# Kernel tuning notes

Hardware: AMD Instinct MI355X
Metric: run time of the kernel (lower is better)

## Reference

```python
import jax, jax.numpy as jnp
import numpy as np
import math

D_MODEL, N_HEADS, D_HEAD = 768, 12, 64
INIT_RANGE = 0.02
ROPE_BASE = 10000.0


def _rope_cos_sin(seq_len, d_head, dtype=jnp.float32):
    # theta_j = base^(-2j/d), positions m -> angles [T, d/2]
    inv_freq = 1.0 / (ROPE_BASE ** (jnp.arange(0, d_head, 2, dtype=jnp.float32) / d_head))
    ang = jnp.arange(seq_len, dtype=jnp.float32)[:, None] * inv_freq[None, :]
    return jnp.cos(ang).astype(dtype), jnp.sin(ang).astype(dtype)


def _apply_rope(x, cos, sin):
    # x: [b, t, h, d]; rotate consecutive (even, odd) pairs as complex numbers
    xr, xi = x[..., 0::2], x[..., 1::2]
    c = cos[None, :, None, :]
    s = sin[None, :, None, :]
    out_r = xr * c - xi * s
    out_i = xr * s + xi * c
    return jnp.stack([out_r, out_i], axis=-1).reshape(x.shape)


def setup_inputs() -> dict:
    key = jax.random.key(0)
    ks = jax.random.split(key, 5)
    B, T = 2, 2048
    x = jax.random.normal(ks[0], (B, T, D_MODEL), dtype=jnp.float32)
    W_Q = INIT_RANGE * jax.random.normal(ks[1], (N_HEADS, D_MODEL, D_HEAD), dtype=jnp.float32)
    W_K = INIT_RANGE * jax.random.normal(ks[2], (N_HEADS, D_MODEL, D_HEAD), dtype=jnp.float32)
    W_V = INIT_RANGE * jax.random.normal(ks[3], (N_HEADS, D_MODEL, D_HEAD), dtype=jnp.float32)
    W_O = INIT_RANGE * jax.random.normal(ks[4], (N_HEADS, D_HEAD, D_MODEL), dtype=jnp.float32)
    b_Q = jnp.zeros((N_HEADS, D_HEAD), dtype=jnp.float32)
    b_K = jnp.zeros((N_HEADS, D_HEAD), dtype=jnp.float32)
    b_V = jnp.zeros((N_HEADS, D_HEAD), dtype=jnp.float32)
    b_O = jnp.zeros((D_MODEL,), dtype=jnp.float32)
    return {"normalized_resid_pre": x, "W_Q": W_Q, "b_Q": b_Q, "W_K": W_K, "b_K": b_K,
            "W_V": W_V, "b_V": b_V, "W_O": W_O, "b_O": b_O}


def reference(normalized_resid_pre, W_Q, b_Q, W_K, b_K, W_V, b_V, W_O, b_O):
    x = normalized_resid_pre
    B, T, _ = x.shape
    cos, sin = _rope_cos_sin(T, D_HEAD, x.dtype)
    Q = jnp.einsum('btc,hcd->bthd', x, W_Q) + b_Q
    K = jnp.einsum('btc,hcd->bthd', x, W_K) + b_K
    V = jnp.einsum('btc,hcd->bthd', x, W_V) + b_V
    Q = _apply_rope(Q, cos, sin)
    K = _apply_rope(K, cos, sin)
    scores = jnp.einsum('bqhd,bkhd->bhqk', Q, K) / math.sqrt(D_HEAD)
    # Faithful to source: tril zeros upper triangle, then all exact zeros -> -inf
    tril = jnp.tril(jnp.ones((T, T), dtype=bool))
    z = jnp.where(tril[None, None], scores, 0.0)
    z = jnp.where(z == 0.0, -jnp.inf, z)
    probs = jax.nn.softmax(z, axis=-1)
    o = jnp.einsum('bhqk,bkhd->bqhd', probs, V)
    return jnp.einsum('bqhd,hdm->bqm', o, W_O) + b_O
```

## Files before the change

### kernel.cpp

```cpp
#include <hip/hip_runtime.h>

typedef unsigned short u16;
typedef unsigned int u32;
typedef short bf16x8 __attribute__((ext_vector_type(8)));
typedef float f32x4 __attribute__((ext_vector_type(4)));
typedef float f32x16 __attribute__((ext_vector_type(16)));

#define MFMA(a, b, c) __builtin_amdgcn_mfma_f32_16x16x32_bf16(a, b, c, 0, 0, 0)
#define MFMA32(a, b, c) __builtin_amdgcn_mfma_f32_32x32x16_bf16(a, b, c, 0, 0, 0)

__device__ __forceinline__ u16 f2bf(float f) {
  unsigned int u = __float_as_uint(f);
  u = (u + 0x7FFFu + ((u >> 16) & 1u)) >> 16;
  return (u16)u;
}

#define GLOAD16(gp, lp)                                                        \
  __builtin_amdgcn_global_load_lds(                                            \
      (const __attribute__((address_space(1))) void*)(gp),                     \
      (__attribute__((address_space(3))) void*)(lp), 16, 0, 0)

__global__ __launch_bounds__(256) void prep_all(
    const float* __restrict__ x, const float* __restrict__ WQ,
    const float* __restrict__ WK, const float* __restrict__ WV,
    const float* __restrict__ WO, float* __restrict__ cost, float* __restrict__ sint,
    u16* __restrict__ xb, u16* __restrict__ Wt, u16* __restrict__ WoT) {
  __shared__ float tile[32][33];
  const int bid = blockIdx.x, tid = threadIdx.x;

  if (bid < 256) {
    int idx = bid * 256 + tid;
    int t = idx >> 5, i = idx & 31;
    float invf = expf(-(float)i * 0.28782313662425572f);
    float ang = (float)t * invf;
    cost[idx] = cosf(ang);
    sint[idx] = sinf(ang);
  } else if (bid < 3328) {
    int i = ((bid - 256) * 256 + tid) * 4;
    float4 v = *(const float4*)(x + i);
    ushort4 o = make_ushort4(f2bf(v.x), f2bf(v.y), f2bf(v.z), f2bf(v.w));
    *(ushort4*)(xb + i) = o;
  } else if (bid < 5056) {
    const int pbid = bid - 3328;
    const int z = pbid / 48, rem = pbid - z * 48;
    const int y = rem / 24, xk = rem - y * 24;
    const int qkv = z / 12, h = z - qkv * 12;
    const float* W = (qkv == 0 ? WQ : qkv == 1 ? WK : WV) + (size_t)h * 768 * 64;
    const int k0 = xk * 32, d0 = y * 32;
    const int tx = tid & 31, ty = tid >> 5;
#pragma unroll
    for (int it = 0; it < 4; it++)
      tile[ty + it * 8][tx] = W[(size_t)(k0 + ty + it * 8) * 64 + d0 + tx];
    __syncthreads();
    u16* out = Wt + (size_t)(qkv * 768 + h * 64 + d0) * 768 + k0;
#pragma unroll
    for (int it = 0; it < 4; it++)
      out[(size_t)(ty + it * 8) * 768 + tx] = f2bf(tile[tx][ty + it * 8]);
  } else {
    const int wbid = bid - 5056;
    const int a0 = (wbid % 24) * 32, m0 = (wbid / 24) * 32;
    const int tx = tid & 31, ty = tid >> 5;
#pragma unroll
    for (int it = 0; it < 4; it++)
      tile[ty + it * 8][tx] = WO[(size_t)(a0 + ty + it * 8) * 768 + m0 + tx];
    __syncthreads();
#pragma unroll
    for (int it = 0; it < 4; it++)
      WoT[(size_t)(m0 + ty + it * 8) * 768 + a0 + tx] = f2bf(tile[tx][ty + it * 8]);
  }
}

__global__ __launch_bounds__(256) void gemm_qkv(
    const u16* __restrict__ A, const u16* __restrict__ Bt,
    const float* __restrict__ bQ, const float* __restrict__ bK, const float* __restrict__ bV,
    const float* __restrict__ cost, const float* __restrict__ sint,
    u16* __restrict__ Qb, u16* __restrict__ Kb, u16* __restrict__ Vt) {
  __shared__ u16 As[3][128 * 32];
  __shared__ u16 Bs[3][96 * 32];
  const int tid = threadIdx.x;
  const int w = tid >> 6, l = tid & 63;
  const int lr = l >> 4, lc = l & 15;
  const int wr = w >> 1, wc = w & 1;

  const int id = blockIdx.x;
  const int xcd = id & 7, idx = id >> 3;
  const int m0 = (xcd * 4 + (idx & 3)) * 128;
  const int n0 = (idx >> 2) * 96;

  f32x4 acc[4][3];
#pragma unroll
  for (int mi = 0; mi < 4; mi++)
#pragma unroll
    for (int ni = 0; ni < 3; ni++) acc[mi][ni] = (f32x4){0.f, 0.f, 0.f, 0.f};

  const int srow = w * 16 + (l >> 2);
  const int sg = (l & 3) ^ ((l >> 3) & 3);
  const u16* ga = A + (size_t)(m0 + srow) * 768 + sg * 8;
  const u16* gb = Bt + (size_t)(n0 + srow) * 768 + sg * 8;
  const u16* gb2 = Bt + (size_t)(n0 + 64 + w * 16 + (l >> 2)) * 768 + sg * 8;

#define GSTAGE(t, bi)                                                     \
  {                                                                       \
    const int kk = (t) * 32;                                              \
    GLOAD16(ga + kk, &As[bi][w * 512]);                                   \
    GLOAD16(ga + kk + (size_t)64 * 768, &As[bi][2048 + w * 512]);         \
    GLOAD16(gb + kk, &Bs[bi][w * 512]);                                   \
    if (w < 2) GLOAD16(gb2 + kk, &Bs[bi][2048 + w * 512]);                \
  }

  const int nt = 24;
  GSTAGE(0, 0);
  GSTAGE(1, 1);

  for (int kt = 0; kt < nt; kt++) {
    if (kt + 1 < nt) {
      if (w < 2) asm volatile("s_waitcnt vmcnt(4)" ::: "memory");
      else       asm volatile("s_waitcnt vmcnt(3)" ::: "memory");
    } else {
      asm volatile("s_waitcnt vmcnt(0)" ::: "memory");
    }
    __builtin_amdgcn_s_barrier();
    __builtin_amdgcn_sched_barrier(0);
    if (kt + 2 < nt) GSTAGE(kt + 2, (kt + 2) % 3);

    const char* as = (const char*)As[kt % 3];
    const char* bs = (const char*)Bs[kt % 3];
    bf16x8 af[4], bfr[3];
#pragma unroll
    for (int mi = 0; mi < 4; mi++) {
      const int row = wr * 64 + mi * 16 + lc;
      af[mi] = *(const bf16x8*)(as + row * 64 + ((lr ^ ((row >> 1) & 3)) << 4));
    }
#pragma unroll
    for (int ni = 0; ni < 3; ni++) {
      const int row = wc * 48 + ni * 16 + lc;
      bfr[ni] = *(const bf16x8*)(bs + row * 64 + ((lr ^ ((row >> 1) & 3)) << 4));
    }
    __builtin_amdgcn_s_setprio(1);
#pragma unroll
    for (int mi = 0; mi < 4; mi++)
#pragma unroll
      for (int ni = 0; ni < 3; ni++)
        acc[mi][ni] = MFMA(af[mi], bfr[ni], acc[mi][ni]);
    __builtin_amdgcn_s_setprio(0);
  }
#undef GSTAGE

#pragma unroll
  for (int mi = 0; mi < 4; mi++) {
#pragma unroll
    for (int ni = 0; ni < 3; ni++) {
      const int col = n0 + wc * 48 + ni * 16 + lc;
      const int rowb = m0 + wr * 64 + mi * 16 + lr * 4;
      const int qkv = col / 768;
      const int rem = col - qkv * 768;
      const int h = rem >> 6, d = rem & 63, fi = d >> 1;
      const float bb = (qkv == 0 ? bQ : qkv == 1 ? bK : bV)[rem];
#pragma unroll
      for (int r = 0; r < 4; r++) {
        const int grow = rowb + r;
        const int t = grow & 2047;
        float v = acc[mi][ni][r] + bb;
        float pv = __shfl_xor(v, 1);
        if (qkv < 2) {
          const float c = cost[t * 32 + fi], s = sint[t * 32 + fi];
          float o = (d & 1) ? (pv * s + v * c) : (v * c - pv * s);
          if (qkv == 0) o *= 0.125f;
          (qkv == 0 ? Qb : Kb)[(size_t)grow * 768 + rem] = f2bf(o);
        } else {
          const int bidx = grow >> 11;
          Vt[((size_t)(bidx * 12 + h) * 64 + d) * 2048 + t] = f2bf(v);
        }
      }
    }
  }
}

__global__ __launch_bounds__(256) void gemm_out(
    const u16* __restrict__ A, const u16* __restrict__ Bt,
    const float* __restrict__ bO, float* __restrict__ Out) {
  __shared__ u16 As[3][64 * 32];
  __shared__ u16 Bs[3][96 * 32];
  const int tid = threadIdx.x;
  const int w = tid >> 6, l = tid & 63;
  const int lr = l >> 4, lc = l & 15;
  const int wr = w >> 1, wc = w & 1;

  const int id = blockIdx.x;
  const int xcd = id & 7, idx = id >> 3;
  const int m0 = (xcd * 8 + (idx & 7)) * 64;
  const int n0 = (idx >> 3) * 96;

  f32x4 acc[2][3];
#pragma unroll
  for (int mi = 0; mi < 2; mi++)
#pragma unroll
    for (int ni = 0; ni < 3; ni++) acc[mi][ni] = (f32x4){0.f, 0.f, 0.f, 0.f};

  const int srow = w * 16 + (l >> 2);
  const int sg = (l & 3) ^ ((l >> 3) & 3);
  const u16* ga = A + (size_t)(m0 + (srow & 63)) * 768 + sg * 8;
  const u16* gb = Bt + (size_t)(n0 + srow) * 768 + sg * 8;
  const u16* gb2 = Bt + (size_t)(n0 + 64 + w * 16 + (l >> 2)) * 768 + sg * 8;

#define GSTAGE(t, bi)                                                   \
  {                                                                     \
    const int kk = (t) * 32;                                            \
    GLOAD16(ga + kk, &As[bi][w * 512]);                                 \
    GLOAD16(gb + kk, &Bs[bi][w * 512]);                                 \
    if (w < 2) GLOAD16(gb2 + kk, &Bs[bi][2048 + w * 512]);              \
  }

  const int nt = 24;
  GSTAGE(0, 0);
  GSTAGE(1, 1);

  for (int kt = 0; kt < nt; kt++) {
    if (kt + 1 < nt) {
      if (w < 2) asm volatile("s_waitcnt vmcnt(3)" ::: "memory");
      else       asm volatile("s_waitcnt vmcnt(2)" ::: "memory");
    } else {
      asm volatile("s_waitcnt vmcnt(0)" ::: "memory");
    }
    __builtin_amdgcn_s_barrier();
    __builtin_amdgcn_sched_barrier(0);
    if (kt + 2 < nt) GSTAGE(kt + 2, (kt + 2) % 3);

    const char* as = (const char*)As[kt % 3];
    const char* bs = (const char*)Bs[kt % 3];
    bf16x8 af[2], bfr[3];
#pragma unroll
    for (int mi = 0; mi < 2; mi++) {
      const int row = wr * 32 + mi * 16 + lc;
      af[mi] = *(const bf16x8*)(as + row * 64 + ((lr ^ ((row >> 1) & 3)) << 4));
    }
#pragma unroll
    for (int ni = 0; ni < 3; ni++) {
      const int row = wc * 48 + ni * 16 + lc;
      bfr[ni] = *(const bf16x8*)(bs + row * 64 + ((lr ^ ((row >> 1) & 3)) << 4));
    }
    __builtin_amdgcn_s_setprio(1);
#pragma unroll
    for (int mi = 0; mi < 2; mi++)
#pragma unroll
      for (int ni = 0; ni < 3; ni++)
        acc[mi][ni] = MFMA(af[mi], bfr[ni], acc[mi][ni]);
    __builtin_amdgcn_s_setprio(0);
  }
#undef GSTAGE

#pragma unroll
  for (int mi = 0; mi < 2; mi++) {
#pragma unroll
    for (int ni = 0; ni < 3; ni++) {
      const int col = n0 + wc * 48 + ni * 16 + lc;
      const int rowb = m0 + wr * 32 + mi * 16 + lr * 4;
      const float bb = bO[col];
#pragma unroll
      for (int r = 0; r < 4; r++) {
        const int grow = rowb + r;
        Out[(size_t)grow * 768 + col] = acc[mi][ni][r] + bb;
      }
    }
  }
}

__global__ __launch_bounds__(256, 2) void attn_kernel(
    const u16* __restrict__ Qb, const u16* __restrict__ Kb,
    const u16* __restrict__ Vt, u16* __restrict__ Ob) {
  __shared__ char Kls[4][8192];
  __shared__ char Vls[4][8192];
  char* scratch = (char*)Kls;

  const int id = blockIdx.x + 16 * blockIdx.y;
  const int s_ = id >> 3;
  const int bh = (id & 7) + 8 * (s_ % 3);
  const int xq = s_ / 3;
  const int b = bh / 12, h = bh - b * 12;
  const int tid = threadIdx.x, w = tid >> 6, l = tid & 63;
  const int lq = l & 31, hi = l >> 5;
  const int qhalf = w & 1, grp = w >> 1;

  const u16* kbase = Kb + (size_t)(b * 2048) * 768 + h * 64;
  const u16* vbase = Vt + (size_t)(bh * 64) * 2048;

  const int r8 = l >> 3;
  const int scol8 = (l & 7) ^ r8;
  const u16* ksrc = kbase + (size_t)(w * 16 + r8) * 768 + scol8 * 8;
  const u16* vsrc = vbase + (size_t)(w * 16 + r8) * 2048 + scol8 * 8;

#define STAGE(t, bi)                                                        \
  {                                                                         \
    const size_t ko = (size_t)(t) * 64 * 768;                               \
    const int vo = (t) * 64;                                                \
    GLOAD16(ksrc + ko,            &Kls[bi][w * 2048]);                      \
    GLOAD16(ksrc + ko + 8 * 768,  &Kls[bi][w * 2048 + 1024]);               \
    GLOAD16(vsrc + vo,            &Vls[bi][w * 2048]);                      \
    GLOAD16(vsrc + vo + 8 * 2048, &Vls[bi][w * 2048 + 1024]);               \
  }

  const int fswz = (lq & 7) << 4;

#pragma unroll 1
  for (int half = 0; half < 2; half++) {
    const int qblk = half == 0 ? 31 - xq : xq;
    const int n = qblk + 1;
    const int nsup = (n + 1) >> 1;

    bf16x8 qf[4];
    {
      const u16* qp = Qb + ((size_t)(b * 2048 + qblk * 64 + qhalf * 32 + lq)) * 768 +
                      h * 64 + hi * 8;
#pragma unroll
      for (int c = 0; c < 4; c++) qf[c] = *(const bf16x8*)(qp + c * 16);
    }

    float m_run = -INFINITY, l_run = 0.f;
    f32x16 acc2[2];
    acc2[0] = (f32x16)0.0f;
    acc2[1] = (f32x16)0.0f;

    STAGE(0, 0);
    if (n > 1) STAGE(1, 1);

    for (int p = 0; p < nsup; p++) {
      const int t0 = 2 * p;
      asm volatile("s_waitcnt vmcnt(0)" ::: "memory");
      __builtin_amdgcn_s_barrier();
      __builtin_amdgcn_sched_barrier(0);
      if (t0 + 2 < n) STAGE(t0 + 2, (t0 + 2) & 3);
      if (t0 + 3 < n) STAGE(t0 + 3, (t0 + 3) & 3);

      const int tile = t0 + grp;
      if (tile < n) {
        const int cur = tile & 3;

        f32x16 s2[2];
        s2[0] = (f32x16)0.0f;
        s2[1] = (f32x16)0.0f;
        __builtin_amdgcn_s_setprio(1);
#pragma unroll
        for (int c = 0; c < 4; c++) {
          const int cb = (c * 32 + hi * 16) ^ fswz;
          bf16x8 kf0 = *(const bf16x8*)(&Kls[cur][lq * 128] + cb);
          bf16x8 kf1 = *(const bf16x8*)(&Kls[cur][(32 + lq) * 128] + cb);
          s2[0] = MFMA32(kf0, qf[c], s2[0]);
          s2[1] = MFMA32(kf1, qf[c], s2[1]);
        }
        __builtin_amdgcn_s_setprio(0);

        if (tile == qblk) {
          const int qrel = qhalf * 32 + lq;
#pragma unroll
          for (int kt2 = 0; kt2 < 2; kt2++)
#pragma unroll
            for (int r = 0; r < 16; r++) {
              const int ko = kt2 * 32 + (r & 3) + 8 * (r >> 2) + 4 * hi;
              if (ko > qrel) s2[kt2][r] = -INFINITY;
            }
        }

        float pm = s2[0][0];
#pragma unroll
        for (int r = 1; r < 16; r++) pm = fmaxf(pm, s2[0][r]);
#pragma unroll
        for (int r = 0; r < 16; r++) pm = fmaxf(pm, s2[1][r]);
        pm = fmaxf(pm, __shfl_xor(pm, 32));

        const bool defer = __all(pm <= m_run + 8.0f);
        if (!defer) {
          const float mn = fmaxf(m_run, pm);
          const float alpha = __expf(m_run - mn);
          m_run = mn;
          l_run *= alpha;
#pragma unroll
          for (int dh = 0; dh < 2; dh++)
#pragma unroll
            for (int r = 0; r < 16; r++) acc2[dh][r] *= alpha;
        }

        float rs = 0.f;
        u32 pk[2][8];
#pragma unroll
        for (int kt2 = 0; kt2 < 2; kt2++)
#pragma unroll
          for (int j = 0; j < 8; j++) {
            float p0 = __expf(s2[kt2][2 * j] - m_run);
            float p1 = __expf(s2[kt2][2 * j + 1] - m_run);
            rs += p0 + p1;
            asm("v_cvt_pk_bf16_f32 %0, %1, %2" : "=v"(pk[kt2][j]) : "v"(p0), "v"(p1));
          }
        l_run += rs;

        union { u32 u[4]; bf16x8 v; } pf[4];
#pragma unroll
        for (int kq = 0; kq < 4; kq++) {
          const int kt2 = kq >> 1, i0 = 4 * (kq & 1);
          u32 a0 = pk[kt2][i0], b0 = pk[kt2][i0 + 2];
          u32 a1 = pk[kt2][i0 + 1], b1 = pk[kt2][i0 + 3];
          asm("v_permlane32_swap_b32 %0, %1" : "+v"(a0), "+v"(b0));
          asm("v_permlane32_swap_b32 %0, %1" : "+v"(a1), "+v"(b1));
          pf[kq].u[0] = a0; pf[kq].u[1] = a1; pf[kq].u[2] = b0; pf[kq].u[3] = b1;
        }

        __builtin_amdgcn_s_setprio(1);
#pragma unroll
        for (int dh = 0; dh < 2; dh++) {
          const char* vr = &Vls[cur][(dh * 32 + lq) * 128];
#pragma unroll
          for (int kq = 0; kq < 4; kq++) {
            bf16x8 vf = *(const bf16x8*)(vr + ((kq * 32 + hi * 16) ^ fswz));
            acc2[dh] = MFMA32(vf, pf[kq].v, acc2[dh]);
          }
        }
        __builtin_amdgcn_s_setprio(0);
      }
    }

    asm volatile("s_waitcnt lgkmcnt(0)" ::: "memory");
    __builtin_amdgcn_s_barrier();
    if (grp == 1) {
      float* sc = (float*)scratch + ((size_t)(w - 2) * 64 + l) * 34;
#pragma unroll
      for (int dh = 0; dh < 2; dh++)
#pragma unroll
        for (int r = 0; r < 16; r++) sc[dh * 16 + r] = acc2[dh][r];
      sc[32] = m_run;
      sc[33] = l_run;
    }
    asm volatile("s_waitcnt lgkmcnt(0)" ::: "memory");
    __builtin_amdgcn_s_barrier();
    if (grp == 0) {
      const float* sc = (const float*)scratch + ((size_t)w * 64 + l) * 34;
      const float m1 = sc[32], l1 = sc[33];
      const float M = fmaxf(m_run, m1);
      const float a0 = __expf(m_run - M);
      const float a1 = __expf(m1 - M);
      const float lm = l_run * a0 + l1 * a1;
      const float lt = lm + __shfl_xor(lm, 32);
      const float inv = 1.0f / lt;
      u16* ob = Ob + ((size_t)(b * 2048 + qblk * 64 + qhalf * 32 + lq)) * 768 + h * 64;
#pragma unroll
      for (int dh = 0; dh < 2; dh++)
#pragma unroll
        for (int g = 0; g < 4; g++) {
          ushort4 o4;
          o4.x = f2bf((acc2[dh][4 * g + 0] * a0 + sc[dh * 16 + 4 * g + 0] * a1) * inv);
          o4.y = f2bf((acc2[dh][4 * g + 1] * a0 + sc[dh * 16 + 4 * g + 1] * a1) * inv);
          o4.z = f2bf((acc2[dh][4 * g + 2] * a0 + sc[dh * 16 + 4 * g + 2] * a1) * inv);
          o4.w = f2bf((acc2[dh][4 * g + 3] * a0 + sc[dh * 16 + 4 * g + 3] * a1) * inv);
          *(ushort4*)(ob + dh * 32 + 8 * g + 4 * hi) = o4;
        }
    }
    asm volatile("s_waitcnt lgkmcnt(0)" ::: "memory");
    __builtin_amdgcn_s_barrier();
  }
#undef STAGE
}


extern "C" void kernel_launch(void* const* d_in, const int* in_sizes, int n_in,
                              void* d_out, int out_size, void* d_ws, size_t ws_size,
                              hipStream_t stream) {
  const float* x  = (const float*)d_in[0];
  const float* WQ = (const float*)d_in[1];
  const float* bQ = (const float*)d_in[2];
  const float* WK = (const float*)d_in[3];
  const float* bK = (const float*)d_in[4];
  const float* WV = (const float*)d_in[5];
  const float* bV = (const float*)d_in[6];
  const float* WO = (const float*)d_in[7];
  const float* bO = (const float*)d_in[8];

  char* ws = (char*)d_ws;
  u16* Xb    = (u16*)(ws + 0);
  u16* Wqkv  = (u16*)(ws + 6291456);
  u16* WoT   = (u16*)(ws + 9830400);
  u16* Qb    = (u16*)(ws + 11010048);
  u16* Kb    = (u16*)(ws + 17301504);
  u16* Vt    = (u16*)(ws + 23592960);
  u16* Ob    = (u16*)(ws + 29884416);
  float* cost = (float*)(ws + 36175872);
  float* sint = (float*)(ws + 36438016);

  prep_all<<<5632, 256, 0, stream>>>(x, WQ, WK, WV, WO, cost, sint, Xb, Wqkv, WoT);

  gemm_qkv<<<768, 256, 0, stream>>>(Xb, Wqkv, bQ, bK, bV, cost, sint, Qb, Kb, Vt);
  attn_kernel<<<dim3(16, 24), 256, 0, stream>>>(Qb, Kb, Vt, Ob);
  gemm_out<<<512, 256, 0, stream>>>(Ob, WoT, bO, (float*)d_out);
}
```

Baseline: 96.03 us.

## Split attention work across 768 smaller blocks with split-KV partials and merge kernel

Restructures causal attention from 384 blocks of 256 threads into 768 blocks of 128 threads. Each block either handles one half of the KV range for a long query tile, writing bf16 partial accumulators plus m/l to workspace, or handles a short query tile directly. A new merge kernel combines the two partials per long tile. Staging moves from a 4-buffer scheme synchronised with a full vmcnt(0) wait to a 3-buffer ring with partial vmcnt waits. The goal is better load balance and more resident blocks, at the cost of an extra launch, partial-result traffic and bf16 rounding of the unnormalised partials.

```diff
diff --git a/kernel.cpp b/kernel.cpp
--- a/kernel.cpp
+++ b/kernel.cpp
@@ -13,6 +13,9 @@
   unsigned int u = __float_as_uint(f);
   u = (u + 0x7FFFu + ((u >> 16) & 1u)) >> 16;
   return (u16)u;
+}
+__device__ __forceinline__ float bf2f(u16 v) {
+  return __uint_as_float(((u32)v) << 16);
 }
 
 #define GLOAD16(gp, lp)                                                        \
@@ -265,197 +268,237 @@
   }
 }
 
-__global__ __launch_bounds__(256, 2) void attn_kernel(
+__device__ __forceinline__ void attn_range(
+    int qtile, int kv0, int kvn, int writePartial,
+    const u16* __restrict__ Qb, const u16* __restrict__ kbase,
+    const u16* __restrict__ vbase, char* Kls0, char* Vls0,
+    int b, int h, int w, int l, char* pbase, u16* __restrict__ Ob) {
+  const int lq = l & 31, hi = l >> 5;
+  const int fswz = (lq & 7) << 4;
+  const int r8 = l >> 3;
+  const int scol8 = (l & 7) ^ r8;
+  const u16* ksrc = kbase + (size_t)(w * 32 + r8) * 768 + scol8 * 8;
+  const u16* vsrc = vbase + (size_t)(w * 32 + r8) * 2048 + scol8 * 8;
+
+#define STG(t, bi)                                                            \
+  {                                                                           \
+    _Pragma("unroll")                                                         \
+    for (int i = 0; i < 4; i++) {                                             \
+      GLOAD16(ksrc + (size_t)(t) * 64 * 768 + (size_t)i * 8 * 768,            \
+              Kls0 + (bi) * 8192 + (w * 32 + i * 8) * 128);                   \
+      GLOAD16(vsrc + (t) * 64 + (size_t)i * 8 * 2048,                         \
+              Vls0 + (bi) * 8192 + (w * 32 + i * 8) * 128);                   \
+    }                                                                         \
+  }
+
+  bf16x8 qf[4];
+  {
+    const u16* qp = Qb + ((size_t)(b * 2048 + qtile * 64 + w * 32 + lq)) * 768 +
+                    h * 64 + hi * 8;
+#pragma unroll
+    for (int c = 0; c < 4; c++) qf[c] = *(const bf16x8*)(qp + c * 16);
+  }
+
+  float m_run = -INFINITY, l_run = 0.f;
+  f32x16 acc2[2];
+  acc2[0] = (f32x16)0.0f;
+  acc2[1] = (f32x16)0.0f;
+
+  STG(kv0, 0);
+  if (kvn - kv0 > 1) STG(kv0 + 1, 1);
+
+  for (int kv = kv0; kv < kvn; kv++) {
+    const int idx = kv - kv0;
+    if (kv + 1 < kvn) asm volatile("s_waitcnt vmcnt(8)" ::: "memory");
+    else              asm volatile("s_waitcnt vmcnt(0)" ::: "memory");
+    __builtin_amdgcn_s_barrier();
+    __builtin_amdgcn_sched_barrier(0);
+    if (kv + 2 < kvn) STG(kv + 2, (idx + 2) % 3);
+
+    const char* kls = Kls0 + (idx % 3) * 8192;
+    const char* vls = Vls0 + (idx % 3) * 8192;
+
+    f32x16 s2[2];
+    s2[0] = (f32x16)0.0f;
+    s2[1] = (f32x16)0.0f;
+    __builtin_amdgcn_s_setprio(1);
+#pragma unroll
+    for (int c = 0; c < 4; c++) {
+      const int cb = (c * 32 + hi * 16) ^ fswz;
+      bf16x8 kf0 = *(const bf16x8*)(kls + lq * 128 + cb);
+      bf16x8 kf1 = *(const bf16x8*)(kls + (32 + lq) * 128 + cb);
+      s2[0] = MFMA32(kf0, qf[c], s2[0]);
+      s2[1] = MFMA32(kf1, qf[c], s2[1]);
+    }
+    __builtin_amdgcn_s_setprio(0);
+
+    if (kv == qtile) {
+      const int qrel = w * 32 + lq;
+#pragma unroll
+      for (int kt2 = 0; kt2 < 2; kt2++)
+#pragma unroll
+        for (int r = 0; r < 16; r++) {
+          const int ko = kt2 * 32 + (r & 3) + 8 * (r >> 2) + 4 * hi;
+          if (ko > qrel) s2[kt2][r] = -INFINITY;
+        }
+    }
+
+    float pm = s2[0][0];
+#pragma unroll
+    for (int r = 1; r < 16; r++) pm = fmaxf(pm, s2[0][r]);
+#pragma unroll
+    for (int r = 0; r < 16; r++) pm = fmaxf(pm, s2[1][r]);
+    pm = fmaxf(pm, __shfl_xor(pm, 32));
+
+    const bool defer = __all(pm <= m_run + 8.0f);
+    if (!defer) {
+      const float mn = fmaxf(m_run, pm);
+      const float alpha = __expf(m_run - mn);
+      m_run = mn;
+      l_run *= alpha;
+#pragma unroll
+      for (int dh = 0; dh < 2; dh++)
+#pragma unroll
+        for (int r = 0; r < 16; r++) acc2[dh][r] *= alpha;
+    }
+
+    float rs = 0.f;
+    u32 pk[2][8];
+#pragma unroll
+    for (int kt2 = 0; kt2 < 2; kt2++)
+#pragma unroll
+      for (int j = 0; j < 8; j++) {
+        float p0 = __expf(s2[kt2][2 * j] - m_run);
+        float p1 = __expf(s2[kt2][2 * j + 1] - m_run);
+        rs += p0 + p1;
+        asm("v_cvt_pk_bf16_f32 %0, %1, %2" : "=v"(pk[kt2][j]) : "v"(p0), "v"(p1));
+      }
+    l_run += rs;
+
+    union { u32 u[4]; bf16x8 v; } pf[4];
+#pragma unroll
+    for (int kq = 0; kq < 4; kq++) {
+      const int kt2 = kq >> 1, i0 = 4 * (kq & 1);
+      u32 a0 = pk[kt2][i0], b0 = pk[kt2][i0 + 2];
+      u32 a1 = pk[kt2][i0 + 1], b1 = pk[kt2][i0 + 3];
+      asm("v_permlane32_swap_b32 %0, %1" : "+v"(a0), "+v"(b0));
+      asm("v_permlane32_swap_b32 %0, %1" : "+v"(a1), "+v"(b1));
+      pf[kq].u[0] = a0; pf[kq].u[1] = a1; pf[kq].u[2] = b0; pf[kq].u[3] = b1;
+    }
+
+    __builtin_amdgcn_s_setprio(1);
+#pragma unroll
+    for (int dh = 0; dh < 2; dh++) {
+      const char* vr = vls + (dh * 32 + lq) * 128;
+#pragma unroll
+      for (int kq = 0; kq < 4; kq++) {
+        bf16x8 vf = *(const bf16x8*)(vr + ((kq * 32 + hi * 16) ^ fswz));
+        acc2[dh] = MFMA32(vf, pf[kq].v, acc2[dh]);
+      }
+    }
+    __builtin_amdgcn_s_setprio(0);
+  }
+#undef STG
+
+  const int t = w * 64 + l;
+  if (writePartial) {
+#pragma unroll
+    for (int g2 = 0; g2 < 8; g2++) {
+      ushort4 o4;
+      o4.x = f2bf(acc2[g2 >> 2][(g2 & 3) * 4 + 0]);
+      o4.y = f2bf(acc2[g2 >> 2][(g2 & 3) * 4 + 1]);
+      o4.z = f2bf(acc2[g2 >> 2][(g2 & 3) * 4 + 2]);
+      o4.w = f2bf(acc2[g2 >> 2][(g2 & 3) * 4 + 3]);
+      *(ushort4*)(pbase + t * 64 + g2 * 8) = o4;
+    }
+    *(float*)(pbase + 8192 + t * 4) = m_run;
+    *(float*)(pbase + 8704 + t * 4) = l_run;
+  } else {
+    const float lt = l_run + __shfl_xor(l_run, 32);
+    const float inv = 1.0f / lt;
+    u16* ob = Ob + ((size_t)(b * 2048 + qtile * 64 + w * 32 + lq)) * 768 + h * 64;
+#pragma unroll
+    for (int dh = 0; dh < 2; dh++)
+#pragma unroll
+      for (int g = 0; g < 4; g++) {
+        ushort4 o4;
+        o4.x = f2bf(acc2[dh][4 * g + 0] * inv);
+        o4.y = f2bf(acc2[dh][4 * g + 1] * inv);
+        o4.z = f2bf(acc2[dh][4 * g + 2] * inv);
+        o4.w = f2bf(acc2[dh][4 * g + 3] * inv);
+        *(ushort4*)(ob + dh * 32 + 8 * g + 4 * hi) = o4;
+      }
+  }
+}
+
+__global__ __launch_bounds__(128) void attn_kernel(
     const u16* __restrict__ Qb, const u16* __restrict__ Kb,
-    const u16* __restrict__ Vt, u16* __restrict__ Ob) {
-  __shared__ char Kls[4][8192];
-  __shared__ char Vls[4][8192];
-  char* scratch = (char*)Kls;
-
-  const int id = blockIdx.x + 16 * blockIdx.y;
+    const u16* __restrict__ Vt, u16* __restrict__ Ob, char* __restrict__ part) {
+  __shared__ char Kls[3][8192];
+  __shared__ char Vls[3][8192];
+  const int id = blockIdx.x;
   const int s_ = id >> 3;
   const int bh = (id & 7) + 8 * (s_ % 3);
-  const int xq = s_ / 3;
+  const int t_ = s_ / 3;
+  const int x = t_ >> 1, side = t_ & 1;
   const int b = bh / 12, h = bh - b * 12;
   const int tid = threadIdx.x, w = tid >> 6, l = tid & 63;
-  const int lq = l & 31, hi = l >> 5;
-  const int qhalf = w & 1, grp = w >> 1;
 
   const u16* kbase = Kb + (size_t)(b * 2048) * 768 + h * 64;
   const u16* vbase = Vt + (size_t)(bh * 64) * 2048;
 
-  const int r8 = l >> 3;
-  const int scol8 = (l & 7) ^ r8;
-  const u16* ksrc = kbase + (size_t)(w * 16 + r8) * 768 + scol8 * 8;
-  const u16* vsrc = vbase + (size_t)(w * 16 + r8) * 2048 + scol8 * 8;
-
-#define STAGE(t, bi)                                                        \
-  {                                                                         \
-    const size_t ko = (size_t)(t) * 64 * 768;                               \
-    const int vo = (t) * 64;                                                \
-    GLOAD16(ksrc + ko,            &Kls[bi][w * 2048]);                      \
-    GLOAD16(ksrc + ko + 8 * 768,  &Kls[bi][w * 2048 + 1024]);               \
-    GLOAD16(vsrc + vo,            &Vls[bi][w * 2048]);                      \
-    GLOAD16(vsrc + vo + 8 * 2048, &Vls[bi][w * 2048 + 1024]);               \
-  }
-
-  const int fswz = (lq & 7) << 4;
-
-#pragma unroll 1
-  for (int half = 0; half < 2; half++) {
-    const int qblk = half == 0 ? 31 - xq : xq;
-    const int n = qblk + 1;
-    const int nsup = (n + 1) >> 1;
-
-    bf16x8 qf[4];
-    {
-      const u16* qp = Qb + ((size_t)(b * 2048 + qblk * 64 + qhalf * 32 + lq)) * 768 +
-                      h * 64 + hi * 8;
-#pragma unroll
-      for (int c = 0; c < 4; c++) qf[c] = *(const bf16x8*)(qp + c * 16);
-    }
-
-    float m_run = -INFINITY, l_run = 0.f;
-    f32x16 acc2[2];
-    acc2[0] = (f32x16)0.0f;
-    acc2[1] = (f32x16)0.0f;
-
-    STAGE(0, 0);
-    if (n > 1) STAGE(1, 1);
-
-    for (int p = 0; p < nsup; p++) {
-      const int t0 = 2 * p;
-      asm volatile("s_waitcnt vmcnt(0)" ::: "memory");
-      __builtin_amdgcn_s_barrier();
-      __builtin_amdgcn_sched_barrier(0);
-      if (t0 + 2 < n) STAGE(t0 + 2, (t0 + 2) & 3);
-      if (t0 + 3 < n) STAGE(t0 + 3, (t0 + 3) & 3);
-
-      const int tile = t0 + grp;
-      if (tile < n) {
-        const int cur = tile & 3;
-
-        f32x16 s2[2];
-        s2[0] = (f32x16)0.0f;
-        s2[1] = (f32x16)0.0f;
-        __builtin_amdgcn_s_setprio(1);
-#pragma unroll
-        for (int c = 0; c < 4; c++) {
-          const int cb = (c * 32 + hi * 16) ^ fswz;
-          bf16x8 kf0 = *(const bf16x8*)(&Kls[cur][lq * 128] + cb);
-          bf16x8 kf1 = *(const bf16x8*)(&Kls[cur][(32 + lq) * 128] + cb);
-          s2[0] = MFMA32(kf0, qf[c], s2[0]);
-          s2[1] = MFMA32(kf1, qf[c], s2[1]);
-        }
-        __builtin_amdgcn_s_setprio(0);
-
-        if (tile == qblk) {
-          const int qrel = qhalf * 32 + lq;
-#pragma unroll
-          for (int kt2 = 0; kt2 < 2; kt2++)
-#pragma unroll
-            for (int r = 0; r < 16; r++) {
-              const int ko = kt2 * 32 + (r & 3) + 8 * (r >> 2) + 4 * hi;
-              if (ko > qrel) s2[kt2][r] = -INFINITY;
-            }
-        }
-
-        float pm = s2[0][0];
-#pragma unroll
-        for (int r = 1; r < 16; r++) pm = fmaxf(pm, s2[0][r]);
-#pragma unroll
-        for (int r = 0; r < 16; r++) pm = fmaxf(pm, s2[1][r]);
-        pm = fmaxf(pm, __shfl_xor(pm, 32));
-
-        const bool defer = __all(pm <= m_run + 8.0f);
-        if (!defer) {
-          const float mn = fmaxf(m_run, pm);
-          const float alpha = __expf(m_run - mn);
-          m_run = mn;
-          l_run *= alpha;
-#pragma unroll
-          for (int dh = 0; dh < 2; dh++)
-#pragma unroll
-            for (int r = 0; r < 16; r++) acc2[dh][r] *= alpha;
-        }
-
-        float rs = 0.f;
-        u32 pk[2][8];
-#pragma unroll
-        for (int kt2 = 0; kt2 < 2; kt2++)
-#pragma unroll
-          for (int j = 0; j < 8; j++) {
-            float p0 = __expf(s2[kt2][2 * j] - m_run);
-            float p1 = __expf(s2[kt2][2 * j + 1] - m_run);
-            rs += p0 + p1;
-            asm("v_cvt_pk_bf16_f32 %0, %1, %2" : "=v"(pk[kt2][j]) : "v"(p0), "v"(p1));
-          }
-        l_run += rs;
-
-        union { u32 u[4]; bf16x8 v; } pf[4];
-#pragma unroll
-        for (int kq = 0; kq < 4; kq++) {
-          const int kt2 = kq >> 1, i0 = 4 * (kq & 1);
-          u32 a0 = pk[kt2][i0], b0 = pk[kt2][i0 + 2];
-          u32 a1 = pk[kt2][i0 + 1], b1 = pk[kt2][i0 + 3];
-          asm("v_permlane32_swap_b32 %0, %1" : "+v"(a0), "+v"(b0));
-          asm("v_permlane32_swap_b32 %0, %1" : "+v"(a1), "+v"(b1));
-          pf[kq].u[0] = a0; pf[kq].u[1] = a1; pf[kq].u[2] = b0; pf[kq].u[3] = b1;
-        }
-
-        __builtin_amdgcn_s_setprio(1);
-#pragma unroll
-        for (int dh = 0; dh < 2; dh++) {
-          const char* vr = &Vls[cur][(dh * 32 + lq) * 128];
-#pragma unroll
-          for (int kq = 0; kq < 4; kq++) {
-            bf16x8 vf = *(const bf16x8*)(vr + ((kq * 32 + hi * 16) ^ fswz));
-            acc2[dh] = MFMA32(vf, pf[kq].v, acc2[dh]);
-          }
-        }
-        __builtin_amdgcn_s_setprio(0);
-      }
-    }
-
+  const int p = bh * 16 + x;
+  const int tileL = 31 - x, nL = 32 - x;
+
+  if (side == 0) {
+    attn_range(tileL, 0, 16, 1, Qb, kbase, vbase, (char*)Kls, (char*)Vls,
+               b, h, w, l, part + (size_t)(2 * p) * 9216, Ob);
+  } else {
+    attn_range(tileL, 16, nL, 1, Qb, kbase, vbase, (char*)Kls, (char*)Vls,
+               b, h, w, l, part + (size_t)(2 * p + 1) * 9216, Ob);
     asm volatile("s_waitcnt lgkmcnt(0)" ::: "memory");
     __builtin_amdgcn_s_barrier();
-    if (grp == 1) {
-      float* sc = (float*)scratch + ((size_t)(w - 2) * 64 + l) * 34;
-#pragma unroll
-      for (int dh = 0; dh < 2; dh++)
-#pragma unroll
-        for (int r = 0; r < 16; r++) sc[dh * 16 + r] = acc2[dh][r];
-      sc[32] = m_run;
-      sc[33] = l_run;
-    }
-    asm volatile("s_waitcnt lgkmcnt(0)" ::: "memory");
-    __builtin_amdgcn_s_barrier();
-    if (grp == 0) {
-      const float* sc = (const float*)scratch + ((size_t)w * 64 + l) * 34;
-      const float m1 = sc[32], l1 = sc[33];
-      const float M = fmaxf(m_run, m1);
-      const float a0 = __expf(m_run - M);
-      const float a1 = __expf(m1 - M);
-      const float lm = l_run * a0 + l1 * a1;
-      const float lt = lm + __shfl_xor(lm, 32);
-      const float inv = 1.0f / lt;
-      u16* ob = Ob + ((size_t)(b * 2048 + qblk * 64 + qhalf * 32 + lq)) * 768 + h * 64;
-#pragma unroll
-      for (int dh = 0; dh < 2; dh++)
-#pragma unroll
-        for (int g = 0; g < 4; g++) {
-          ushort4 o4;
-          o4.x = f2bf((acc2[dh][4 * g + 0] * a0 + sc[dh * 16 + 4 * g + 0] * a1) * inv);
-          o4.y = f2bf((acc2[dh][4 * g + 1] * a0 + sc[dh * 16 + 4 * g + 1] * a1) * inv);
-          o4.z = f2bf((acc2[dh][4 * g + 2] * a0 + sc[dh * 16 + 4 * g + 2] * a1) * inv);
-          o4.w = f2bf((acc2[dh][4 * g + 3] * a0 + sc[dh * 16 + 4 * g + 3] * a1) * inv);
-          *(ushort4*)(ob + dh * 32 + 8 * g + 4 * hi) = o4;
-        }
-    }
-    asm volatile("s_waitcnt lgkmcnt(0)" ::: "memory");
-    __builtin_amdgcn_s_barrier();
-  }
-#undef STAGE
+    attn_range(x, 0, x + 1, 0, Qb, kbase, vbase, (char*)Kls, (char*)Vls,
+               b, h, w, l, nullptr, Ob);
+  }
+}
+
+__global__ __launch_bounds__(128) void attn_merge(
+    const char* __restrict__ part, u16* __restrict__ Ob) {
+  const int p = blockIdx.x;
+  const int t = threadIdx.x;
+  const int w = t >> 6, l = t & 63;
+  const int lq = l & 31, hi = l >> 5;
+  const char* p0 = part + (size_t)(2 * p) * 9216;
+  const char* p1 = p0 + 9216;
+
+  const float m0 = *(const float*)(p0 + 8192 + t * 4);
+  const float l0 = *(const float*)(p0 + 8704 + t * 4);
+  const float m1 = *(const float*)(p1 + 8192 + t * 4);
+  const float l1 = *(const float*)(p1 + 8704 + t * 4);
+  const float M = fmaxf(m0, m1);
+  const float a0 = __expf(m0 - M), a1 = __expf(m1 - M);
+  const float lm = l0 * a0 + l1 * a1;
+  const float lt = lm + __shfl_xor(lm, 32);
+  const float inv = 1.0f / lt;
+
+  const int bh = p >> 4, x = p & 15;
+  const int b = bh / 12, h = bh - b * 12;
+  const int q = (31 - x) * 64 + w * 32 + lq;
+  u16* ob = Ob + ((size_t)(b * 2048 + q)) * 768 + h * 64;
+
+#pragma unroll
+  for (int g2 = 0; g2 < 8; g2++) {
+    ushort4 u0 = *(const ushort4*)(p0 + t * 64 + g2 * 8);
+    ushort4 u1 = *(const ushort4*)(p1 + t * 64 + g2 * 8);
+    ushort4 o4;
+    o4.x = f2bf((bf2f(u0.x) * a0 + bf2f(u1.x) * a1) * inv);
+    o4.y = f2bf((bf2f(u0.y) * a0 + bf2f(u1.y) * a1) * inv);
+    o4.z = f2bf((bf2f(u0.z) * a0 + bf2f(u1.z) * a1) * inv);
+    o4.w = f2bf((bf2f(u0.w) * a0 + bf2f(u1.w) * a1) * inv);
+    const int dh = g2 >> 2, g = g2 & 3;
+    *(ushort4*)(ob + dh * 32 + 8 * g + 4 * hi) = o4;
+  }
 }
 
 
@@ -482,10 +525,12 @@
   u16* Ob    = (u16*)(ws + 29884416);
   float* cost = (float*)(ws + 36175872);
   float* sint = (float*)(ws + 36438016);
+  char* part  = ws + 0;
 
   prep_all<<<5632, 256, 0, stream>>>(x, WQ, WK, WV, WO, cost, sint, Xb, Wqkv, WoT);
 
   gemm_qkv<<<768, 256, 0, stream>>>(Xb, Wqkv, bQ, bK, bV, cost, sint, Qb, Kb, Vt);
-  attn_kernel<<<dim3(16, 24), 256, 0, stream>>>(Qb, Kb, Vt, Ob);
+  attn_kernel<<<768, 128, 0, stream>>>(Qb, Kb, Vt, Ob, part);
+  attn_merge<<<384, 128, 0, stream>>>(part, Ob);
   gemm_out<<<512, 256, 0, stream>>>(Ob, WoT, bO, (float*)d_out);
 }
```

Measured after the change: 100.3 us. 1.04x slower.

## Process paired causal query tiles concurrently sharing one KV stream

Applied to the files above, without the earlier changes.

The attention block now splits its four waves across two query tiles (31-x and x) at the same time, instead of processing them one after another with the KV range split between wave groups. Both tiles share a single streamed pass over KV tiles through a 3-deep LDS ring with partial vmcnt waits. This removes the cross-group softmax merge through LDS scratch and the second prologue. The cost is that the waves on the short tile sit idle once past their diagonal, and launch_bounds no longer asks for 2 blocks per CU.

```diff
diff --git a/kernel.cpp b/kernel.cpp
--- a/kernel.cpp
+++ b/kernel.cpp
@@ -265,21 +265,23 @@
   }
 }
 
-__global__ __launch_bounds__(256, 2) void attn_kernel(
+__global__ __launch_bounds__(256) void attn_kernel(
     const u16* __restrict__ Qb, const u16* __restrict__ Kb,
     const u16* __restrict__ Vt, u16* __restrict__ Ob) {
-  __shared__ char Kls[4][8192];
-  __shared__ char Vls[4][8192];
-  char* scratch = (char*)Kls;
-
-  const int id = blockIdx.x + 16 * blockIdx.y;
+  __shared__ char Kls[3][8192];
+  __shared__ char Vls[3][8192];
+
+  const int id = blockIdx.x;
   const int s_ = id >> 3;
   const int bh = (id & 7) + 8 * (s_ % 3);
-  const int xq = s_ / 3;
+  const int x = s_ / 3;
   const int b = bh / 12, h = bh - b * 12;
   const int tid = threadIdx.x, w = tid >> 6, l = tid & 63;
   const int lq = l & 31, hi = l >> 5;
-  const int qhalf = w & 1, grp = w >> 1;
+  const int qhalf = w & 1;
+  const int qtile = (w >> 1) ? x : 31 - x;
+  const int myN = qtile + 1;
+  const int n = 32 - x;
 
   const u16* kbase = Kb + (size_t)(b * 2048) * 768 + h * 64;
   const u16* vbase = Vt + (size_t)(bh * 64) * 2048;
@@ -301,161 +303,131 @@
 
   const int fswz = (lq & 7) << 4;
 
-#pragma unroll 1
-  for (int half = 0; half < 2; half++) {
-    const int qblk = half == 0 ? 31 - xq : xq;
-    const int n = qblk + 1;
-    const int nsup = (n + 1) >> 1;
-
-    bf16x8 qf[4];
-    {
-      const u16* qp = Qb + ((size_t)(b * 2048 + qblk * 64 + qhalf * 32 + lq)) * 768 +
-                      h * 64 + hi * 8;
-#pragma unroll
-      for (int c = 0; c < 4; c++) qf[c] = *(const bf16x8*)(qp + c * 16);
-    }
-
-    float m_run = -INFINITY, l_run = 0.f;
-    f32x16 acc2[2];
-    acc2[0] = (f32x16)0.0f;
-    acc2[1] = (f32x16)0.0f;
-
-    STAGE(0, 0);
-    if (n > 1) STAGE(1, 1);
-
-    for (int p = 0; p < nsup; p++) {
-      const int t0 = 2 * p;
-      asm volatile("s_waitcnt vmcnt(0)" ::: "memory");
-      __builtin_amdgcn_s_barrier();
-      __builtin_amdgcn_sched_barrier(0);
-      if (t0 + 2 < n) STAGE(t0 + 2, (t0 + 2) & 3);
-      if (t0 + 3 < n) STAGE(t0 + 3, (t0 + 3) & 3);
-
-      const int tile = t0 + grp;
-      if (tile < n) {
-        const int cur = tile & 3;
-
-        f32x16 s2[2];
-        s2[0] = (f32x16)0.0f;
-        s2[1] = (f32x16)0.0f;
-        __builtin_amdgcn_s_setprio(1);
-#pragma unroll
-        for (int c = 0; c < 4; c++) {
-          const int cb = (c * 32 + hi * 16) ^ fswz;
-          bf16x8 kf0 = *(const bf16x8*)(&Kls[cur][lq * 128] + cb);
-          bf16x8 kf1 = *(const bf16x8*)(&Kls[cur][(32 + lq) * 128] + cb);
-          s2[0] = MFMA32(kf0, qf[c], s2[0]);
-          s2[1] = MFMA32(kf1, qf[c], s2[1]);
+  bf16x8 qf[4];
+  {
+    const u16* qp = Qb + ((size_t)(b * 2048 + qtile * 64 + qhalf * 32 + lq)) * 768 +
+                    h * 64 + hi * 8;
+#pragma unroll
+    for (int c = 0; c < 4; c++) qf[c] = *(const bf16x8*)(qp + c * 16);
+  }
+
+  float m_run = -INFINITY, l_run = 0.f;
+  f32x16 acc2[2];
+  acc2[0] = (f32x16)0.0f;
+  acc2[1] = (f32x16)0.0f;
+
+  STAGE(0, 0);
+  if (n > 1) STAGE(1, 1);
+
+  for (int kv = 0; kv < n; kv++) {
+    if (kv + 1 < n) asm volatile("s_waitcnt vmcnt(4)" ::: "memory");
+    else            asm volatile("s_waitcnt vmcnt(0)" ::: "memory");
+    __builtin_amdgcn_s_barrier();
+    __builtin_amdgcn_sched_barrier(0);
+    if (kv + 2 < n) STAGE(kv + 2, (kv + 2) % 3);
+
+    if (kv < myN) {
+      const int cur = kv % 3;
+      const char* kls = Kls[cur];
+      const char* vls = Vls[cur];
+
+      f32x16 s2[2];
+      s2[0] = (f32x16)0.0f;
+      s2[1] = (f32x16)0.0f;
+      __builtin_amdgcn_s_setprio(1);
+#pragma unroll
+      for (int c = 0; c < 4; c++) {
+        const int cb = (c * 32 + hi * 16) ^ fswz;
+        bf16x8 kf0 = *(const bf16x8*)(kls + lq * 128 + cb);
+        bf16x8 kf1 = *(const bf16x8*)(kls + (32 + lq) * 128 + cb);
+        s2[0] = MFMA32(kf0, qf[c], s2[0]);
+        s2[1] = MFMA32(kf1, qf[c], s2[1]);
+      }
+      __builtin_amdgcn_s_setprio(0);
+
+      if (kv == qtile) {
+        const int qrel = qhalf * 32 + lq;
+#pragma unroll
+        for (int kt2 = 0; kt2 < 2; kt2++)
+#pragma unroll
+          for (int r = 0; r < 16; r++) {
+            const int ko = kt2 * 32 + (r & 3) + 8 * (r >> 2) + 4 * hi;
+            if (ko > qrel) s2[kt2][r] = -INFINITY;
+          }
+      }
+
+      float pm = s2[0][0];
+#pragma unroll
+      for (int r = 1; r < 16; r++) pm = fmaxf(pm, s2[0][r]);
+#pragma unroll
+      for (int r = 0; r < 16; r++) pm = fmaxf(pm, s2[1][r]);
+      pm = fmaxf(pm, __shfl_xor(pm, 32));
+
+      const bool defer = __all(pm <= m_run + 8.0f);
+      if (!defer) {
+        const float mn = fmaxf(m_run, pm);
+        const float alpha = __expf(m_run - mn);
+        m_run = mn;
+        l_run *= alpha;
+#pragma unroll
+        for (int dh = 0; dh < 2; dh++)
+#pragma unroll
+          for (int r = 0; r < 16; r++) acc2[dh][r] *= alpha;
+      }
+
+      float rs = 0.f;
+      u32 pk[2][8];
+#pragma unroll
+      for (int kt2 = 0; kt2 < 2; kt2++)
+#pragma unroll
+        for (int j = 0; j < 8; j++) {
+          float p0 = __expf(s2[kt2][2 * j] - m_run);
+          float p1 = __expf(s2[kt2][2 * j + 1] - m_run);
+          rs += p0 + p1;
+          asm("v_cvt_pk_bf16_f32 %0, %1, %2" : "=v"(pk[kt2][j]) : "v"(p0), "v"(p1));
         }
-        __builtin_amdgcn_s_setprio(0);
-
-        if (tile == qblk) {
-          const int qrel = qhalf * 32 + lq;
-#pragma unroll
-          for (int kt2 = 0; kt2 < 2; kt2++)
-#pragma unroll
-            for (int r = 0; r < 16; r++) {
-              const int ko = kt2 * 32 + (r & 3) + 8 * (r >> 2) + 4 * hi;
-              if (ko > qrel) s2[kt2][r] = -INFINITY;
-            }
+      l_run += rs;
+
+      union { u32 u[4]; bf16x8 v; } pf[4];
+#pragma unroll
+      for (int kq = 0; kq < 4; kq++) {
+        const int kt2 = kq >> 1, i0 = 4 * (kq & 1);
+        u32 a0 = pk[kt2][i0], b0 = pk[kt2][i0 + 2];
+        u32 a1 = pk[kt2][i0 + 1], b1 = pk[kt2][i0 + 3];
+        asm("v_permlane32_swap_b32 %0, %1" : "+v"(a0), "+v"(b0));
+        asm("v_permlane32_swap_b32 %0, %1" : "+v"(a1), "+v"(b1));
+        pf[kq].u[0] = a0; pf[kq].u[1] = a1; pf[kq].u[2] = b0; pf[kq].u[3] = b1;
+      }
+
+      __builtin_amdgcn_s_setprio(1);
+#pragma unroll
+      for (int dh = 0; dh < 2; dh++) {
+        const char* vr = vls + (dh * 32 + lq) * 128;
+#pragma unroll
+        for (int kq = 0; kq < 4; kq++) {
+          bf16x8 vf = *(const bf16x8*)(vr + ((kq * 32 + hi * 16) ^ fswz));
+          acc2[dh] = MFMA32(vf, pf[kq].v, acc2[dh]);
         }
-
-        float pm = s2[0][0];
-#pragma unroll
-        for (int r = 1; r < 16; r++) pm = fmaxf(pm, s2[0][r]);
-#pragma unroll
-        for (int r = 0; r < 16; r++) pm = fmaxf(pm, s2[1][r]);
-        pm = fmaxf(pm, __shfl_xor(pm, 32));
-
-        const bool defer = __all(pm <= m_run + 8.0f);
-        if (!defer) {
-          const float mn = fmaxf(m_run, pm);
-          const float alpha = __expf(m_run - mn);
-          m_run = mn;
-          l_run *= alpha;
-#pragma unroll
-          for (int dh = 0; dh < 2; dh++)
-#pragma unroll
-            for (int r = 0; r < 16; r++) acc2[dh][r] *= alpha;
-        }
-
-        float rs = 0.f;
-        u32 pk[2][8];
-#pragma unroll
-        for (int kt2 = 0; kt2 < 2; kt2++)
-#pragma unroll
-          for (int j = 0; j < 8; j++) {
-            float p0 = __expf(s2[kt2][2 * j] - m_run);
-            float p1 = __expf(s2[kt2][2 * j + 1] - m_run);
-            rs += p0 + p1;
-            asm("v_cvt_pk_bf16_f32 %0, %1, %2" : "=v"(pk[kt2][j]) : "v"(p0), "v"(p1));
-          }
-        l_run += rs;
-
-        union { u32 u[4]; bf16x8 v; } pf[4];
-#pragma unroll
-        for (int kq = 0; kq < 4; kq++) {
-          const int kt2 = kq >> 1, i0 = 4 * (kq & 1);
-          u32 a0 = pk[kt2][i0], b0 = pk[kt2][i0 + 2];
-          u32 a1 = pk[kt2][i0 + 1], b1 = pk[kt2][i0 + 3];
-          asm("v_permlane32_swap_b32 %0, %1" : "+v"(a0), "+v"(b0));
-          asm("v_permlane32_swap_b32 %0, %1" : "+v"(a1), "+v"(b1));
-          pf[kq].u[0] = a0; pf[kq].u[1] = a1; pf[kq].u[2] = b0; pf[kq].u[3] = b1;
-        }
-
-        __builtin_amdgcn_s_setprio(1);
-#pragma unroll
-        for (int dh = 0; dh < 2; dh++) {
-          const char* vr = &Vls[cur][(dh * 32 + lq) * 128];
-#pragma unroll
-          for (int kq = 0; kq < 4; kq++) {
-            bf16x8 vf = *(const bf16x8*)(vr + ((kq * 32 + hi * 16) ^ fswz));
-            acc2[dh] = MFMA32(vf, pf[kq].v, acc2[dh]);
-          }
-        }
-        __builtin_amdgcn_s_setprio(0);
-      }
-    }
-
-    asm volatile("s_waitcnt lgkmcnt(0)" ::: "memory");
-    __builtin_amdgcn_s_barrier();
-    if (grp == 1) {
-      float* sc = (float*)scratch + ((size_t)(w - 2) * 64 + l) * 34;
-#pragma unroll
-      for (int dh = 0; dh < 2; dh++)
-#pragma unroll
-        for (int r = 0; r < 16; r++) sc[dh * 16 + r] = acc2[dh][r];
-      sc[32] = m_run;
-      sc[33] = l_run;
-    }
-    asm volatile("s_waitcnt lgkmcnt(0)" ::: "memory");
-    __builtin_amdgcn_s_barrier();
-    if (grp == 0) {
-      const float* sc = (const float*)scratch + ((size_t)w * 64 + l) * 34;
-      const float m1 = sc[32], l1 = sc[33];
-      const float M = fmaxf(m_run, m1);
-      const float a0 = __expf(m_run - M);
-      const float a1 = __expf(m1 - M);
-      const float lm = l_run * a0 + l1 * a1;
-      const float lt = lm + __shfl_xor(lm, 32);
-      const float inv = 1.0f / lt;
-      u16* ob = Ob + ((size_t)(b * 2048 + qblk * 64 + qhalf * 32 + lq)) * 768 + h * 64;
-#pragma unroll
-      for (int dh = 0; dh < 2; dh++)
-#pragma unroll
-        for (int g = 0; g < 4; g++) {
-          ushort4 o4;
-          o4.x = f2bf((acc2[dh][4 * g + 0] * a0 + sc[dh * 16 + 4 * g + 0] * a1) * inv);
-          o4.y = f2bf((acc2[dh][4 * g + 1] * a0 + sc[dh * 16 + 4 * g + 1] * a1) * inv);
-          o4.z = f2bf((acc2[dh][4 * g + 2] * a0 + sc[dh * 16 + 4 * g + 2] * a1) * inv);
-          o4.w = f2bf((acc2[dh][4 * g + 3] * a0 + sc[dh * 16 + 4 * g + 3] * a1) * inv);
-          *(ushort4*)(ob + dh * 32 + 8 * g + 4 * hi) = o4;
-        }
-    }
-    asm volatile("s_waitcnt lgkmcnt(0)" ::: "memory");
-    __builtin_amdgcn_s_barrier();
+      }
+      __builtin_amdgcn_s_setprio(0);
+    }
   }
 #undef STAGE
+
+  const float lt = l_run + __shfl_xor(l_run, 32);
+  const float inv = 1.0f / lt;
+  u16* ob = Ob + ((size_t)(b * 2048 + qtile * 64 + qhalf * 32 + lq)) * 768 + h * 64;
+#pragma unroll
+  for (int dh = 0; dh < 2; dh++)
+#pragma unroll
+    for (int g = 0; g < 4; g++) {
+      ushort4 o4;
+      o4.x = f2bf(acc2[dh][4 * g + 0] * inv);
+      o4.y = f2bf(acc2[dh][4 * g + 1] * inv);
+      o4.z = f2bf(acc2[dh][4 * g + 2] * inv);
+      o4.w = f2bf(acc2[dh][4 * g + 3] * inv);
+      *(ushort4*)(ob + dh * 32 + 8 * g + 4 * hi) = o4;
+    }
 }
 
 
@@ -486,6 +458,6 @@
   prep_all<<<5632, 256, 0, stream>>>(x, WQ, WK, WV, WO, cost, sint, Xb, Wqkv, WoT);
 
   gemm_qkv<<<768, 256, 0, stream>>>(Xb, Wqkv, bQ, bK, bV, cost, sint, Qb, Kb, Vt);
-  attn_kernel<<<dim3(16, 24), 256, 0, stream>>>(Qb, Kb, Vt, Ob);
+  attn_kernel<<<384, 256, 0, stream>>>(Qb, Kb, Vt, Ob);
   gemm_out<<<512, 256, 0, stream>>>(Ob, WoT, bO, (float*)d_out);
 }
```

Measured after the change: 109.9 us. +14.5%, slower.
